# Performance work log

Hardware: AMD Instinct MI355X
Metric: run time of the kernel (lower is better)

## Reference

```python
import jax, jax.numpy as jnp
import numpy as np

B, N, F, H1, H2, NC = 1024, 64, 1024, 256, 128, 128
ALPHA = 0.2   # LeakyReLU slope
BN_EPS = 1e-5


def setup_inputs() -> dict:
    key = jax.random.key(0)
    ks = jax.random.split(key, 20)
    d = {}
    d["x"] = jax.random.normal(ks[0], (B, 1, F), dtype=jnp.float32)
    d["neighbor"] = jax.random.normal(ks[1], (B, N, 1, F), dtype=jnp.float32)
    # GraphAttn layer 1 params
    d["W1"] = jax.random.normal(ks[2], (H1, F), dtype=jnp.float32) / np.sqrt(F)
    d["b1"] = jnp.zeros((H1,), dtype=jnp.float32)
    d["a11"] = jax.random.normal(ks[3], (H1,), dtype=jnp.float32) / np.sqrt(H1)
    d["a12"] = jax.random.normal(ks[4], (H1,), dtype=jnp.float32) / np.sqrt(H1)
    d["g1"] = jnp.ones((), dtype=jnp.float32)   # BatchNorm1d(1) weight (scalar)
    d["be1"] = jnp.zeros((), dtype=jnp.float32)  # BatchNorm1d(1) bias
    # GraphAttn layer 2 params
    d["W2"] = jax.random.normal(ks[5], (H2, H1), dtype=jnp.float32) / np.sqrt(H1)
    d["b2"] = jnp.zeros((H2,), dtype=jnp.float32)
    d["a21"] = jax.random.normal(ks[6], (H2,), dtype=jnp.float32) / np.sqrt(H2)
    d["a22"] = jax.random.normal(ks[7], (H2,), dtype=jnp.float32) / np.sqrt(H2)
    d["g2"] = jnp.ones((), dtype=jnp.float32)
    d["be2"] = jnp.zeros((), dtype=jnp.float32)
    # final classifier
    d["Wl"] = jax.random.normal(ks[8], (NC, H2), dtype=jnp.float32) / np.sqrt(H2)
    d["bl"] = jnp.zeros((NC,), dtype=jnp.float32)
    return d


def _l2norm_c(t):
    # torch nf.normalize default: p=2, dim=1 -> here the singleton channel axis (-2)
    n = jnp.sqrt(jnp.sum(t * t, axis=-2, keepdims=True))
    return t / jnp.maximum(n, 1e-12)


def _gat_layer(x, nb, W, b, a_self, a_nb):
    # x: [B,1,Fin], nb: [B,N,1,Fin]
    xh = jnp.einsum('bcf,hf->bch', x, W) + b        # [B,1,H]
    nbh = jnp.einsum('bncf,hf->bnch', nb, W) + b    # [B,N,1,H]
    # att1(x[i]) + att2(neighbor[i]) -> scores over N (C==1 squeezed)
    s = (jnp.einsum('bch,h->bc', xh, a_self)[:, None, :]
         + jnp.einsum('bnch,h->bnc', nbh, a_nb))[..., 0]   # [B,N]
    A = jax.nn.softmax(jax.nn.leaky_relu(s, ALPHA), axis=1)  # softmax over neighbors
    out = jnp.einsum('bn,bnch->bch', A, nbh)        # [B,1,H]
    return out, nbh


def _bn_relu(t, g, b, axes):
    # BatchNorm1d(1) in training mode: stats over all non-channel dims of the tensor
    m = jnp.mean(t, axis=axes, keepdims=True)
    v = jnp.mean(jnp.square(t - m), axis=axes, keepdims=True)
    return jax.nn.relu(g * (t - m) * jax.lax.rsqrt(v + BN_EPS) + b)


def reference(x, neighbor, W1, b1, a11, a12, g1, be1,
              W2, b2, a21, a22, g2, be2, Wl, bl):
    x = _l2norm_c(x)
    nb = _l2norm_c(neighbor)
    x, nb = _gat_layer(x, nb, W1, b1, a11, a12)
    # acvt1 applied to x [B,1,H1] (stats over B,H) and to each neighbor tensor
    # [N,1,H1] separately (per-sample stats -> axes (1,3) of [B,N,1,H1])
    x = _bn_relu(x, g1, be1, axes=(0, 2))
    nb = _bn_relu(nb, g1, be1, axes=(1, 3))
    x, nb = _gat_layer(x, nb, W2, b2, a21, a22)
    x = _bn_relu(x, g2, be2, axes=(0, 2))
    # Flatten -> Dropout(p=0) -> Linear
    logits = jnp.einsum('bh,ch->bc', x.reshape(x.shape[0], -1), Wl) + bl
    return logits
```

## Files before the change

kernel.cpp:

```cpp
#include <hip/hip_runtime.h>
#include <hip/hip_bf16.h>
#include <stdint.h>

#define B_    1024
#define N_    64
#define F_    1024
#define H1_   256
#define H2_   128
#define NC_   128
#define ALPHA 0.2f
#define BN_EPS 1e-5f

typedef __attribute__((ext_vector_type(4))) float  f32x4;
typedef __attribute__((ext_vector_type(8))) __bf16 bf16x8;
typedef __attribute__((ext_vector_type(4))) __bf16 bf16x4;

__device__ inline float sign_ref(float v) {
    float s = copysignf(1.0f, v);
    return (fabsf(v) >= 1e-12f) ? s : v * 1e12f;
}

__device__ __forceinline__ void gload_lds16(const void* g, void* l) {
    auto gp = reinterpret_cast<const __attribute__((address_space(1))) void*>(
        reinterpret_cast<uintptr_t>(g));
    auto lp = reinterpret_cast<__attribute__((address_space(3))) void*>(
        reinterpret_cast<uintptr_t>(l));
    __builtin_amdgcn_global_load_lds(gp, lp, 16, 0, 0);
}

__device__ inline float blk_reduce(float v, float* buf) {
    #pragma unroll
    for (int o = 32; o > 0; o >>= 1) v += __shfl_xor(v, o, 64);
    __syncthreads();
    const int wave = threadIdx.x >> 6, lane = threadIdx.x & 63;
    if (lane == 0) buf[wave] = v;
    __syncthreads();
    float r = 0.f;
    if (threadIdx.x == 0) {
        const int nw = blockDim.x >> 6;
        for (int i = 0; i < nw; ++i) r += buf[i];
    }
    return r;
}

__global__ __launch_bounds__(256) void k_prep(
    const float* __restrict__ W1, const float* __restrict__ W2,
    const float* __restrict__ b1, const float* __restrict__ a11,
    const float* __restrict__ a12, const float* __restrict__ b2,
    const float* __restrict__ a21, const float* __restrict__ a22,
    __bf16* __restrict__ W1b, __bf16* __restrict__ W2b,
    float* __restrict__ w1a, float* __restrict__ w2a,
    float* __restrict__ w2a22, float* __restrict__ cscal)
{
    __shared__ float rbuf[8];
    const int blk = blockIdx.x, tid = threadIdx.x;
    if (blk < 256) {
        const int i0 = blk * 1024 + tid * 4;
        float4 v = *(const float4*)(W1 + i0);
        bf16x4 p = { (__bf16)v.x, (__bf16)v.y, (__bf16)v.z, (__bf16)v.w };
        *(bf16x4*)(W1b + i0) = p;
    } else if (blk < 288) {
        const int i0 = (blk - 256) * 1024 + tid * 4;
        float4 v = *(const float4*)(W2 + i0);
        bf16x4 p = { (__bf16)v.x, (__bf16)v.y, (__bf16)v.z, (__bf16)v.w };
        *(bf16x4*)(W2b + i0) = p;
    } else if (blk < 292) {
        const int f = (blk - 288) * 256 + tid;
        float s1 = 0.f;
        #pragma unroll 8
        for (int h = 0; h < H1_; ++h) s1 += W1[h * F_ + f] * a11[h];
        w1a[f] = s1;
    } else if (blk == 292) {
        float s1 = 0.f, s2 = 0.f;
        #pragma unroll 8
        for (int h = 0; h < H2_; ++h) {
            const float w = W2[h * H1_ + tid];
            s1 += w * a21[h]; s2 += w * a22[h];
        }
        w2a[tid] = s1; w2a22[tid] = s2;
    } else {
        float v1 = b1[tid] * a11[tid];
        float v2 = (tid < H2_) ? b2[tid] * a21[tid] : 0.f;
        float v3 = (tid < H2_) ? b2[tid] * a22[tid] : 0.f;
        float r1 = blk_reduce(v1, rbuf);
        float r2 = blk_reduce(v2, rbuf);
        float r3 = blk_reduce(v3, rbuf);
        if (tid == 0) { cscal[0] = r1; cscal[1] = r2; cscal[2] = r3; }
    }
}

__global__ __launch_bounds__(256, 1) void k_gemm1(
    const float* __restrict__ A, const __bf16* __restrict__ Bw,
    const float* __restrict__ bias, __bf16* __restrict__ C,
    const float* __restrict__ x, const float* __restrict__ w1a,
    const float* __restrict__ a12, const float* __restrict__ w2a22,
    const float* __restrict__ cscal, const float* __restrict__ g1p,
    const float* __restrict__ be1p,
    float* __restrict__ out1, float* __restrict__ alpha1,
    float* __restrict__ beta1, float* __restrict__ psum1,
    float* __restrict__ psq1, float* __restrict__ spart)
{
    constexpr int BM = 128, BN = 256, BK = 64, K = F_;
    constexpr int LDA = BK + 8;
    __shared__ __attribute__((aligned(16))) char smem[BM * LDA * 2 + BN * BK * 2];
    __bf16* As = (__bf16*)smem;
    __bf16* Bs = (__bf16*)(smem + BM * LDA * 2);
    __bf16* Cs = Bs;
    __shared__ float a12s[H1_];
    __shared__ float w2a22s[H1_];
    __shared__ float sv[N_];
    __shared__ float rbuf[8];
    __shared__ float fscal[4];

    const int tid = threadIdx.x;
    const int wave = tid >> 6, lane = tid & 63;
    const int wm = wave & 1, wn = wave >> 1;
    const int rowin = lane & 15, kq = lane >> 4;
    const size_t m0 = (size_t)blockIdx.x * BM;
    const size_t b0 = (size_t)blockIdx.x * 2;

    {
        const float* xb = x + b0 * F_;
        float p0 = 0.f, p1 = 0.f;
        #pragma unroll
        for (int i = 0; i < 4; ++i) {
            const float wa = w1a[tid + i * 256];
            p0 += sign_ref(xb[tid + i * 256]) * wa;
            p1 += sign_ref(xb[F_ + tid + i * 256]) * wa;
        }
        a12s[tid] = a12[tid]; w2a22s[tid] = w2a22[tid];
        float r0 = blk_reduce(p0, rbuf);
        float r1 = blk_reduce(p1, rbuf);
        if (tid == 0) {
            const float c1 = cscal[0];
            fscal[0] = r0 + c1; fscal[1] = r1 + c1;
        }
    }

    f32x4 acc[4][8] = {};

    const int cqA = tid & 15, r0A = tid >> 4;
    const float* Abase = A + m0 * K + cqA * 4;

    for (int k0 = 0; k0 < K; k0 += BK) {
        #pragma unroll
        for (int it = 0; it < 8; ++it) {
            const int s = it * 256 + tid;
            const int r = s >> 3;
            const int c8 = (s & 7) ^ (r & 7);
            gload_lds16(Bw + (size_t)r * K + k0 + c8 * 8, Bs + s * 8);
        }
        #pragma unroll
        for (int rr = 0; rr < 8; ++rr) {
            const int r = r0A + rr * 16;
            float4 v = *(const float4*)(Abase + (size_t)r * K + k0);
            bf16x4 p = { (__bf16)sign_ref(v.x), (__bf16)sign_ref(v.y),
                         (__bf16)sign_ref(v.z), (__bf16)sign_ref(v.w) };
            *(bf16x4*)&As[r * LDA + cqA * 4] = p;
        }
        __syncthreads();
        #pragma unroll
        for (int ks = 0; ks < 2; ++ks) {
            bf16x8 af[4], bv[8];
            #pragma unroll
            for (int mi = 0; mi < 4; ++mi)
                af[mi] = *(const bf16x8*)&As[(wm * 64 + mi * 16 + rowin) * LDA + ks * 32 + kq * 8];
            #pragma unroll
            for (int ni = 0; ni < 8; ++ni) {
                const int r = wn * 128 + ni * 16 + rowin;
                const int c = (ks * 4 + kq) ^ (r & 7);
                bv[ni] = *(const bf16x8*)&Bs[(r * 8 + c) * 8];
            }
            #pragma unroll
            for (int mi = 0; mi < 4; ++mi)
                #pragma unroll
                for (int ni = 0; ni < 8; ++ni)
                    acc[mi][ni] = __builtin_amdgcn_mfma_f32_16x16x32_bf16(
                        af[mi], bv[ni], acc[mi][ni], 0, 0, 0);
        }
        __syncthreads();
    }
    const int cr0 = (lane >> 4) * 4, cc = lane & 15;
    for (int half = 0; half < 2; ++half) {
        if (wm == half) {
            #pragma unroll
            for (int ni = 0; ni < 8; ++ni) {
                const int col = wn * 128 + ni * 16 + cc;
                const float bs = bias[col];
                #pragma unroll
                for (int mi = 0; mi < 4; ++mi)
                    #pragma unroll
                    for (int i = 0; i < 4; ++i)
                        Cs[(mi * 16 + cr0 + i) * 256 + col] =
                            (__bf16)(acc[mi][ni][i] + bs);
            }
        }
        __syncthreads();
        #pragma unroll
        for (int it = 0; it < 8; ++it) {
            const int s = it * 256 + tid;
            const size_t row = m0 + half * 64 + (s >> 5);
            *(bf16x8*)(C + row * 256 + (s & 31) * 8) = *(const bf16x8*)&Cs[s * 8];
        }
        __syncthreads();

        const size_t b = b0 + half;
        {
            const int n = tid >> 2, q = tid & 3;
            float p = 0.f;
            for (int i = 0; i < 64; ++i) {
                const int h = q * 64 + ((i + tid) & 63);
                p += (float)Cs[n * 256 + h] * a12s[h];
            }
            p += __shfl_xor(p, 1); p += __shfl_xor(p, 2);
            if (q == 0) { float s = fscal[half] + p; sv[n] = s > 0.f ? s : ALPHA * s; }
        }
        __syncthreads();
        if (tid < 64) {
            float s = sv[tid], m = s;
            #pragma unroll
            for (int o = 1; o < 64; o <<= 1) m = fmaxf(m, __shfl_xor(m, o));
            float e = __expf(s - m), t = e;
            #pragma unroll
            for (int o = 1; o < 64; o <<= 1) t += __shfl_xor(t, o);
            sv[tid] = e / t;
        }
        __syncthreads();
        float o1 = 0.f, ss = 0.f, sq = 0.f;
        for (int n2 = 0; n2 < N_; ++n2) {
            const float v = (float)Cs[n2 * 256 + tid];
            o1 += sv[n2] * v; ss += v; sq += v * v;
        }
        out1[b * H1_ + tid] = o1;
        {
            const float rs = blk_reduce(ss, rbuf);
            const float rq = blk_reduce(sq, rbuf);
            if (tid == 0) {
                const float inv = 1.f / (float)(N_ * H1_);
                const float mean = rs * inv, var = rq * inv - mean * mean;
                const float a = (*g1p) * rsqrtf(var + BN_EPS);
                const float bb = (*be1p) - a * mean;
                alpha1[b] = a; beta1[b] = bb;
                fscal[2] = a; fscal[3] = bb;
            }
            const float rsx = blk_reduce(o1, rbuf);
            const float rqx = blk_reduce(o1 * o1, rbuf);
            if (tid == 0) { psum1[b] = rsx; psq1[b] = rqx; }
        }
        __syncthreads();
        {
            const float al_ = fscal[2], be_ = fscal[3];
            const int n = tid >> 2, q = tid & 3;
            float p = 0.f;
            for (int i = 0; i < 64; ++i) {
                const int h = q * 64 + ((i + tid) & 63);
                const float v = (float)Cs[n * 256 + h];
                p += fmaxf(fmaf(al_, v, be_), 0.f) * w2a22s[h];
            }
            p += __shfl_xor(p, 1); p += __shfl_xor(p, 2);
            if (q == 0) spart[b * N_ + n] = p;
        }
        __syncthreads();
    }
}

__global__ __launch_bounds__(256) void k_back(
    const __bf16* __restrict__ nbh1, const float* __restrict__ out1,
    const float* __restrict__ alpha1, const float* __restrict__ beta1,
    const float* __restrict__ psum1, const float* __restrict__ psq1,
    const float* __restrict__ g1p, const float* __restrict__ be1p,
    const float* __restrict__ w2a, const float* __restrict__ spart,
    const float* __restrict__ cscal, const __bf16* __restrict__ W2b,
    const float* __restrict__ b2,
    float* __restrict__ out2, float* __restrict__ psum2,
    float* __restrict__ psq2)
{
    __shared__ __attribute__((aligned(16))) __bf16 tile[N_ * H1_];
    __shared__ float w2as[H1_];
    __shared__ float sv[N_];
    __shared__ float g2s[H1_ + 8];
    __shared__ float hpart[H2_];
    __shared__ float rbuf[8];
    __shared__ float scal[3];

    const int b = blockIdx.x, tid = threadIdx.x;

    const __bf16* src = nbh1 + (size_t)b * N_ * H1_;
    #pragma unroll
    for (int it = 0; it < 8; ++it)
        gload_lds16(src + (it * 256 + tid) * 8, tile + (it * 256 + tid) * 8);
    w2as[tid] = w2a[tid];
    const float o1 = out1[(size_t)b * H1_ + tid];
    const float al = alpha1[b], be = beta1[b];

    {
        float s = 0.f, q = 0.f;
        for (int i = tid; i < B_; i += 256) { s += psum1[i]; q += psq1[i]; }
        const float gs = blk_reduce(s, rbuf);
        const float gq = blk_reduce(q, rbuf);
        if (tid == 0) {
            const float n = (float)(B_ * H1_);
            const float mean = gs / n, var = gq / n - mean * mean;
            const float a = (*g1p) * rsqrtf(var + BN_EPS);
            scal[0] = a; scal[1] = (*be1p) - a * mean;
        }
    }
    __syncthreads();

    {
        const float x2 = fmaxf(fmaf(scal[0], o1, scal[1]), 0.f);
        const float r = blk_reduce(x2 * w2as[tid], rbuf);
        if (tid == 0) scal[2] = r + cscal[1] + cscal[2];
    }
    __syncthreads();

    if (tid < 64) {
        float s = scal[2] + spart[(size_t)b * N_ + tid];
        s = s > 0.f ? s : ALPHA * s;
        float m = s;
        #pragma unroll
        for (int o = 1; o < 64; o <<= 1) m = fmaxf(m, __shfl_xor(m, o));
        float e = __expf(s - m), t = e;
        #pragma unroll
        for (int o = 1; o < 64; o <<= 1) t += __shfl_xor(t, o);
        sv[tid] = e / t;
    }
    __syncthreads();

    {
        float g = 0.f;
        for (int n2 = 0; n2 < N_; ++n2) {
            const float v = (float)tile[n2 * H1_ + tid];
            g += sv[n2] * fmaxf(fmaf(al, v, be), 0.f);
        }
        g2s[tid + (tid >> 5)] = g;
    }
    __syncthreads();

    #pragma unroll 4
    for (int j = 0; j < 16; ++j) {
        const int idx = j * 256 + tid;
        const int h = idx >> 5, k8 = idx & 31;
        const bf16x8 w = ((const bf16x8*)W2b)[idx];
        float p = 0.f;
        #pragma unroll
        for (int i = 0; i < 8; ++i) {
            const int k = k8 * 8 + i;
            p += (float)w[i] * g2s[k + (k >> 5)];
        }
        p += __shfl_xor(p, 1); p += __shfl_xor(p, 2); p += __shfl_xor(p, 4);
        p += __shfl_xor(p, 8); p += __shfl_xor(p, 16);
        if ((tid & 31) == 0) hpart[h] = p;
    }
    __syncthreads();
    {
        float o2 = 0.f;
        if (tid < H2_) o2 = hpart[tid] + b2[tid];
        const float rs2 = blk_reduce(o2, rbuf);
        const float rq2 = blk_reduce(o2 * o2, rbuf);
        if (tid < H2_) out2[(size_t)b * H2_ + tid] = o2;
        if (tid == 0) { psum2[b] = rs2; psq2[b] = rq2; }
    }
}

__global__ __launch_bounds__(128) void k_fin(
    const float* __restrict__ out2, const float* __restrict__ psum2,
    const float* __restrict__ psq2, const float* __restrict__ g2p,
    const float* __restrict__ be2p, const float* __restrict__ Wl,
    const float* __restrict__ bl, float* __restrict__ logits)
{
    __shared__ float xr[H2_];
    __shared__ float Ws[NC_][H2_ + 1];
    __shared__ float axbx[2];
    __shared__ float rbuf[8];
    const int b = blockIdx.x, tid = threadIdx.x;
    {
        float s = 0.f, q = 0.f;
        for (int i = tid; i < B_; i += 128) { s += psum2[i]; q += psq2[i]; }
        const float gs = blk_reduce(s, rbuf);
        const float gq = blk_reduce(q, rbuf);
        if (tid == 0) {
            const float n = (float)(B_ * H2_);
            const float mean = gs / n, var = gq / n - mean * mean;
            const float a = (*g2p) * rsqrtf(var + BN_EPS);
            axbx[0] = a; axbx[1] = (*be2p) - a * mean;
        }
    }
    for (int i = tid; i < NC_ * H2_ / 4; i += 128) {
        float4 v = ((const float4*)Wl)[i];
        const int r = i >> 5, c = (i & 31) * 4;
        Ws[r][c] = v.x; Ws[r][c + 1] = v.y; Ws[r][c + 2] = v.z; Ws[r][c + 3] = v.w;
    }
    __syncthreads();
    xr[tid] = fmaxf(fmaf(axbx[0], out2[(size_t)b * H2_ + tid], axbx[1]), 0.f);
    __syncthreads();
    float acc = bl[tid];
    #pragma unroll 4
    for (int h = 0; h < H2_; ++h) acc += xr[h] * Ws[tid][h];
    logits[(size_t)b * NC_ + tid] = acc;
}

extern "C" void kernel_launch(void* const* d_in, const int* in_sizes, int n_in,
                              void* d_out, int out_size, void* d_ws, size_t ws_size,
                              hipStream_t stream)
{
    const float* x   = (const float*)d_in[0];
    const float* nb  = (const float*)d_in[1];
    const float* W1  = (const float*)d_in[2];
    const float* b1  = (const float*)d_in[3];
    const float* a11 = (const float*)d_in[4];
    const float* a12 = (const float*)d_in[5];
    const float* g1  = (const float*)d_in[6];
    const float* be1 = (const float*)d_in[7];
    const float* W2  = (const float*)d_in[8];
    const float* b2  = (const float*)d_in[9];
    const float* a21 = (const float*)d_in[10];
    const float* a22 = (const float*)d_in[11];
    const float* g2  = (const float*)d_in[12];
    const float* be2 = (const float*)d_in[13];
    const float* Wl  = (const float*)d_in[14];
    const float* bl  = (const float*)d_in[15];
    float* logits = (float*)d_out;

    size_t off = 0;
    auto alc = [&](size_t bytes) {
        void* p = (char*)d_ws + off;
        off = (off + bytes + 255) & ~(size_t)255;
        return p;
    };
    __bf16* W1b   = (__bf16*)alc((size_t)H1_ * F_ * 2);
    __bf16* W2b   = (__bf16*)alc((size_t)H2_ * H1_ * 2);
    float* w1a    = (float*)alc(F_ * 4);
    float* w2a    = (float*)alc(H1_ * 4);
    float* w2a22  = (float*)alc(H1_ * 4);
    float* cscal  = (float*)alc(3 * 4);
    float* alpha1 = (float*)alc(B_ * 4);
    float* beta1  = (float*)alc(B_ * 4);
    float* psum1  = (float*)alc(B_ * 4);
    float* psq1   = (float*)alc(B_ * 4);
    float* psum2  = (float*)alc(B_ * 4);
    float* psq2   = (float*)alc(B_ * 4);
    float* spart  = (float*)alc((size_t)B_ * N_ * 4);
    float* out1   = (float*)alc((size_t)B_ * H1_ * 4);
    float* out2   = (float*)alc((size_t)B_ * H2_ * 4);
    __bf16* nbh1  = (__bf16*)alc((size_t)B_ * N_ * H1_ * 2);

    k_prep<<<294, 256, 0, stream>>>(W1, W2, b1, a11, a12, b2, a21, a22,
                                    W1b, W2b, w1a, w2a, w2a22, cscal);
    k_gemm1<<<(B_ * N_) / 128, 256, 0, stream>>>(
        nb, W1b, b1, nbh1, x, w1a, a12, w2a22, cscal, g1, be1,
        out1, alpha1, beta1, psum1, psq1, spart);
    k_back<<<B_, 256, 0, stream>>>(nbh1, out1, alpha1, beta1, psum1, psq1,
                                   g1, be1, w2a, spart, cscal, W2b, b2,
                                   out2, psum2, psq2);
    k_fin<<<B_, 128, 0, stream>>>(out2, psum2, psq2, g2, be2, Wl, bl, logits);
}
```

Measured before the change: 515.6 us.

## Shrink gemm1 tile to one batch element per block for two blocks per CU

The first GEMM block now covers 64 rows (one batch sample) instead of 128, with each wave owning a 64-column slice of the 256-wide output. The accumulator count halves and launch bounds now request two blocks per CU, so the grid doubles to 1024 blocks. The fused epilogue (attention softmax, BN statistics, layer-2 score partials) loses its two-half loop. The aim is more occupancy and better load balance, at the cost of loading the full W1 tile twice as often per output row and lower MFMA reuse per B-fragment load.

New measurement: 467.6 us. 1.1x faster.

```diff
diff --git a/kernel.cpp b/kernel.cpp
--- a/kernel.cpp
+++ b/kernel.cpp
@@ -89,7 +89,7 @@
     }
 }
 
-__global__ __launch_bounds__(256, 1) void k_gemm1(
+__global__ __launch_bounds__(256, 2) void k_gemm1(
     const float* __restrict__ A, const __bf16* __restrict__ Bw,
     const float* __restrict__ bias, __bf16* __restrict__ C,
     const float* __restrict__ x, const float* __restrict__ w1a,
@@ -100,9 +100,9 @@
     float* __restrict__ beta1, float* __restrict__ psum1,
     float* __restrict__ psq1, float* __restrict__ spart)
 {
-    constexpr int BM = 128, BN = 256, BK = 64, K = F_;
+    constexpr int BM = 64, BK = 64, K = F_;
     constexpr int LDA = BK + 8;
-    __shared__ __attribute__((aligned(16))) char smem[BM * LDA * 2 + BN * BK * 2];
+    __shared__ __attribute__((aligned(16))) char smem[BM * LDA * 2 + 256 * BK * 2];
     __bf16* As = (__bf16*)smem;
     __bf16* Bs = (__bf16*)(smem + BM * LDA * 2);
     __bf16* Cs = Bs;
@@ -114,33 +114,24 @@
 
     const int tid = threadIdx.x;
     const int wave = tid >> 6, lane = tid & 63;
-    const int wm = wave & 1, wn = wave >> 1;
     const int rowin = lane & 15, kq = lane >> 4;
-    const size_t m0 = (size_t)blockIdx.x * BM;
-    const size_t b0 = (size_t)blockIdx.x * 2;
-
-    {
-        const float* xb = x + b0 * F_;
-        float p0 = 0.f, p1 = 0.f;
-        #pragma unroll
-        for (int i = 0; i < 4; ++i) {
-            const float wa = w1a[tid + i * 256];
-            p0 += sign_ref(xb[tid + i * 256]) * wa;
-            p1 += sign_ref(xb[F_ + tid + i * 256]) * wa;
-        }
+    const size_t b = blockIdx.x;
+
+    {
+        const float* xb = x + b * F_;
+        float p0 = 0.f;
+        #pragma unroll
+        for (int i = 0; i < 4; ++i)
+            p0 += sign_ref(xb[tid + i * 256]) * w1a[tid + i * 256];
         a12s[tid] = a12[tid]; w2a22s[tid] = w2a22[tid];
         float r0 = blk_reduce(p0, rbuf);
-        float r1 = blk_reduce(p1, rbuf);
-        if (tid == 0) {
-            const float c1 = cscal[0];
-            fscal[0] = r0 + c1; fscal[1] = r1 + c1;
-        }
-    }
-
-    f32x4 acc[4][8] = {};
+        if (tid == 0) fscal[0] = r0 + cscal[0];
+    }
+
+    f32x4 acc[4][4] = {};
 
     const int cqA = tid & 15, r0A = tid >> 4;
-    const float* Abase = A + m0 * K + cqA * 4;
+    const float* Abase = A + b * (size_t)BM * K + cqA * 4;
 
     for (int k0 = 0; k0 < K; k0 += BK) {
         #pragma unroll
@@ -151,7 +142,7 @@
             gload_lds16(Bw + (size_t)r * K + k0 + c8 * 8, Bs + s * 8);
         }
         #pragma unroll
-        for (int rr = 0; rr < 8; ++rr) {
+        for (int rr = 0; rr < 4; ++rr) {
             const int r = r0A + rr * 16;
             float4 v = *(const float4*)(Abase + (size_t)r * K + k0);
             bf16x4 p = { (__bf16)sign_ref(v.x), (__bf16)sign_ref(v.y),
@@ -161,106 +152,98 @@
         __syncthreads();
         #pragma unroll
         for (int ks = 0; ks < 2; ++ks) {
-            bf16x8 af[4], bv[8];
+            bf16x8 af[4], bv[4];
             #pragma unroll
             for (int mi = 0; mi < 4; ++mi)
-                af[mi] = *(const bf16x8*)&As[(wm * 64 + mi * 16 + rowin) * LDA + ks * 32 + kq * 8];
+                af[mi] = *(const bf16x8*)&As[(mi * 16 + rowin) * LDA + ks * 32 + kq * 8];
             #pragma unroll
-            for (int ni = 0; ni < 8; ++ni) {
-                const int r = wn * 128 + ni * 16 + rowin;
+            for (int ni = 0; ni < 4; ++ni) {
+                const int r = wave * 64 + ni * 16 + rowin;
                 const int c = (ks * 4 + kq) ^ (r & 7);
                 bv[ni] = *(const bf16x8*)&Bs[(r * 8 + c) * 8];
             }
             #pragma unroll
             for (int mi = 0; mi < 4; ++mi)
                 #pragma unroll
-                for (int ni = 0; ni < 8; ++ni)
+                for (int ni = 0; ni < 4; ++ni)
                     acc[mi][ni] = __builtin_amdgcn_mfma_f32_16x16x32_bf16(
                         af[mi], bv[ni], acc[mi][ni], 0, 0, 0);
         }
         __syncthreads();
     }
+
     const int cr0 = (lane >> 4) * 4, cc = lane & 15;
-    for (int half = 0; half < 2; ++half) {
-        if (wm == half) {
+    #pragma unroll
+    for (int ni = 0; ni < 4; ++ni) {
+        const int col = wave * 64 + ni * 16 + cc;
+        const float bs = bias[col];
+        #pragma unroll
+        for (int mi = 0; mi < 4; ++mi)
             #pragma unroll
-            for (int ni = 0; ni < 8; ++ni) {
-                const int col = wn * 128 + ni * 16 + cc;
-                const float bs = bias[col];
-                #pragma unroll
-                for (int mi = 0; mi < 4; ++mi)
-                    #pragma unroll
-                    for (int i = 0; i < 4; ++i)
-                        Cs[(mi * 16 + cr0 + i) * 256 + col] =
-                            (__bf16)(acc[mi][ni][i] + bs);
-            }
-        }
-        __syncthreads();
-        #pragma unroll
-        for (int it = 0; it < 8; ++it) {
-            const int s = it * 256 + tid;
-            const size_t row = m0 + half * 64 + (s >> 5);
-            *(bf16x8*)(C + row * 256 + (s & 31) * 8) = *(const bf16x8*)&Cs[s * 8];
-        }
-        __syncthreads();
-
-        const size_t b = b0 + half;
-        {
-            const int n = tid >> 2, q = tid & 3;
-            float p = 0.f;
-            for (int i = 0; i < 64; ++i) {
-                const int h = q * 64 + ((i + tid) & 63);
-                p += (float)Cs[n * 256 + h] * a12s[h];
-            }
-            p += __shfl_xor(p, 1); p += __shfl_xor(p, 2);
-            if (q == 0) { float s = fscal[half] + p; sv[n] = s > 0.f ? s : ALPHA * s; }
-        }
-        __syncthreads();
-        if (tid < 64) {
-            float s = sv[tid], m = s;
-            #pragma unroll
-            for (int o = 1; o < 64; o <<= 1) m = fmaxf(m, __shfl_xor(m, o));
-            float e = __expf(s - m), t = e;
-            #pragma unroll
-            for (int o = 1; o < 64; o <<= 1) t += __shfl_xor(t, o);
-            sv[tid] = e / t;
-        }
-        __syncthreads();
-        float o1 = 0.f, ss = 0.f, sq = 0.f;
-        for (int n2 = 0; n2 < N_; ++n2) {
-            const float v = (float)Cs[n2 * 256 + tid];
-            o1 += sv[n2] * v; ss += v; sq += v * v;
-        }
-        out1[b * H1_ + tid] = o1;
-        {
-            const float rs = blk_reduce(ss, rbuf);
-            const float rq = blk_reduce(sq, rbuf);
-            if (tid == 0) {
-                const float inv = 1.f / (float)(N_ * H1_);
-                const float mean = rs * inv, var = rq * inv - mean * mean;
-                const float a = (*g1p) * rsqrtf(var + BN_EPS);
-                const float bb = (*be1p) - a * mean;
-                alpha1[b] = a; beta1[b] = bb;
-                fscal[2] = a; fscal[3] = bb;
-            }
-            const float rsx = blk_reduce(o1, rbuf);
-            const float rqx = blk_reduce(o1 * o1, rbuf);
-            if (tid == 0) { psum1[b] = rsx; psq1[b] = rqx; }
-        }
-        __syncthreads();
-        {
-            const float al_ = fscal[2], be_ = fscal[3];
-            const int n = tid >> 2, q = tid & 3;
-            float p = 0.f;
-            for (int i = 0; i < 64; ++i) {
-                const int h = q * 64 + ((i + tid) & 63);
-                const float v = (float)Cs[n * 256 + h];
-                p += fmaxf(fmaf(al_, v, be_), 0.f) * w2a22s[h];
-            }
-            p += __shfl_xor(p, 1); p += __shfl_xor(p, 2);
-            if (q == 0) spart[b * N_ + n] = p;
-        }
-        __syncthreads();
+            for (int i = 0; i < 4; ++i)
+                Cs[(mi * 16 + cr0 + i) * 256 + col] = (__bf16)(acc[mi][ni][i] + bs);
+    }
+    __syncthreads();
+    #pragma unroll
+    for (int it = 0; it < 8; ++it) {
+        const int s = it * 256 + tid;
+        *(bf16x8*)(C + (b * 64 + (s >> 5)) * 256 + (s & 31) * 8) =
+            *(const bf16x8*)&Cs[s * 8];
+    }
+    {
+        const int n = tid >> 2, q = tid & 3;
+        float p = 0.f;
+        for (int i = 0; i < 64; ++i) {
+            const int h = q * 64 + ((i + tid) & 63);
+            p += (float)Cs[n * 256 + h] * a12s[h];
+        }
+        p += __shfl_xor(p, 1); p += __shfl_xor(p, 2);
+        if (q == 0) { float s = fscal[0] + p; sv[n] = s > 0.f ? s : ALPHA * s; }
+    }
+    __syncthreads();
+    if (tid < 64) {
+        float s = sv[tid], m = s;
+        #pragma unroll
+        for (int o = 1; o < 64; o <<= 1) m = fmaxf(m, __shfl_xor(m, o));
+        float e = __expf(s - m), t = e;
+        #pragma unroll
+        for (int o = 1; o < 64; o <<= 1) t += __shfl_xor(t, o);
+        sv[tid] = e / t;
+    }
+    __syncthreads();
+    float o1 = 0.f, ss = 0.f, sq = 0.f;
+    for (int n2 = 0; n2 < N_; ++n2) {
+        const float v = (float)Cs[n2 * 256 + tid];
+        o1 += sv[n2] * v; ss += v; sq += v * v;
+    }
+    out1[b * H1_ + tid] = o1;
+    {
+        const float rs = blk_reduce(ss, rbuf);
+        const float rq = blk_reduce(sq, rbuf);
+        if (tid == 0) {
+            const float inv = 1.f / (float)(N_ * H1_);
+            const float mean = rs * inv, var = rq * inv - mean * mean;
+            const float a = (*g1p) * rsqrtf(var + BN_EPS);
+            const float bb = (*be1p) - a * mean;
+            alpha1[b] = a; beta1[b] = bb;
+            fscal[2] = a; fscal[3] = bb;
+        }
+        const float rsx = blk_reduce(o1, rbuf);
+        const float rqx = blk_reduce(o1 * o1, rbuf);
+        if (tid == 0) { psum1[b] = rsx; psq1[b] = rqx; }
+    }
+    __syncthreads();
+    {
+        const float al_ = fscal[2], be_ = fscal[3];
+        const int n = tid >> 2, q = tid & 3;
+        float p = 0.f;
+        for (int i = 0; i < 64; ++i) {
+            const int h = q * 64 + ((i + tid) & 63);
+            const float v = (float)Cs[n * 256 + h];
+            p += fmaxf(fmaf(al_, v, be_), 0.f) * w2a22s[h];
+        }
+        p += __shfl_xor(p, 1); p += __shfl_xor(p, 2);
+        if (q == 0) spart[b * N_ + n] = p;
     }
 }
 
@@ -447,7 +430,7 @@
 
     k_prep<<<294, 256, 0, stream>>>(W1, W2, b1, a11, a12, b2, a21, a22,
                                     W1b, W2b, w1a, w2a, w2a22, cscal);
-    k_gemm1<<<(B_ * N_) / 128, 256, 0, stream>>>(
+    k_gemm1<<<B_, 256, 0, stream>>>(
         nb, W1b, b1, nbh1, x, w1a, a12, w2a22, cscal, g1, be1,
         out1, alpha1, beta1, psum1, psq1, spart);
     k_back<<<B_, 256, 0, stream>>>(nbh1, out1, alpha1, beta1, psum1, psq1,
```
